# Optimization experiments

Hardware: AMD Instinct MI355X
Metric: run time of the kernel (lower is better)

Reference implementation:

```python
import jax, jax.numpy as jnp
import numpy as np

D_MODEL = 256; D_STATE = 64; D_CONV = 4; EXPAND = 2; HEADDIM = 64; CHUNK = 64
D_INNER = EXPAND * D_MODEL          # 512
NHEADS = D_INNER // HEADDIM         # 8
D_IN_PROJ = 2 * D_INNER + 2 * D_STATE + NHEADS   # 1160
CONV_DIM = D_INNER + 2 * D_STATE    # 640
OBS_DIM = 3; T = 4096; BK = 32; K = 4


def setup_inputs() -> dict:
    key = jax.random.key(0)
    ks = jax.random.split(key, 8)
    f = jnp.float32
    return {
        "obs": jax.random.normal(ks[0], (T, BK, OBS_DIM), f),
        "W_in": jax.random.normal(ks[1], (D_MODEL, OBS_DIM), f) * 0.1,
        "b_in": jnp.zeros((D_MODEL,), f),
        "in_proj_w": jax.random.normal(ks[2], (D_IN_PROJ, D_MODEL), f) * 0.02,
        "conv_w": jax.random.normal(ks[3], (CONV_DIM, D_CONV), f) * 0.2,
        "conv_b": jnp.zeros((CONV_DIM,), f),
        "dt_bias": jax.random.normal(ks[4], (NHEADS,), f) * 0.1,
        "A_log": jnp.log(jnp.arange(1, NHEADS + 1, dtype=f)),
        "D_param": jnp.ones((NHEADS,), f),
        "norm_w": jnp.ones((D_INNER,), f),
        "out_proj_w": jax.random.normal(ks[5], (D_MODEL, D_INNER), f) * 0.02,
        "head": jnp.zeros((1,), f),
        "log_tau": jnp.zeros((1,), f),
        "k": K,
    }


def segsum(x):
    """Stable segment-sum: x (..., T) -> (..., T, T) lower-triangular cumulative sums."""
    L = x.shape[-1]
    x = jnp.broadcast_to(x[..., None], (*x.shape, L))
    x = jnp.where(jnp.tril(jnp.ones((L, L), bool), -1), x, 0.0)
    s = jnp.cumsum(x, axis=-2)
    return jnp.where(jnp.tril(jnp.ones((L, L), bool), 0), s, -jnp.inf)


def ssd(x, A, B, C, chunk):
    """Mamba2 SSD. x:(b,l,h,p) A:(b,l,h) B,C:(b,l,n). Returns y:(b,l,h,p), final state."""
    b, l, h, p = x.shape
    c = l // chunk
    x = x.reshape(b, c, chunk, h, p)
    A = A.reshape(b, c, chunk, h).transpose(0, 3, 1, 2)        # (b,h,c,l)
    B = B.reshape(b, c, chunk, -1)
    C = C.reshape(b, c, chunk, -1)
    A_cs = jnp.cumsum(A, axis=-1)                              # (b,h,c,l)
    Lmat = jnp.exp(segsum(A))                                  # (b,h,c,l,s)
    Y_diag = jnp.einsum('bcln,bcsn,bhcls,bcshp->bclhp', C, B, Lmat, x)
    decay_states = jnp.exp(A_cs[..., -1:] - A_cs)              # (b,h,c,l)
    states = jnp.einsum('bcln,bhcl,bclhp->bchpn', B, decay_states, x)
    states = jnp.concatenate([jnp.zeros_like(states[:, :1]), states], axis=1)
    decay_chunk = jnp.exp(segsum(jnp.pad(A_cs[..., -1], ((0, 0), (0, 0), (1, 0)))))
    new_states = jnp.einsum('bhzc,bchpn->bzhpn', decay_chunk, states)
    states, final = new_states[:, :-1], new_states[:, -1]
    Y_off = jnp.einsum('bcln,bchpn,bhcl->bclhp', C, states, jnp.exp(A_cs))
    return (Y_diag + Y_off).reshape(b, l, h, p), final


def reference(obs, W_in, b_in, in_proj_w, conv_w, conv_b, dt_bias, A_log, D_param,
              norm_w, out_proj_w, head, log_tau, k):
    Tt, Bk, _ = obs.shape
    x = obs @ W_in.T + b_in                        # (T,Bk,d_model)  input linear
    u = jnp.transpose(x, (1, 0, 2))                # (Bk,T,d_model)
    zxbcdt = u @ in_proj_w.T                       # (Bk,T,d_in_proj)
    z = zxbcdt[..., :D_INNER]
    xBC = zxbcdt[..., D_INNER:D_INNER + CONV_DIM]
    dt = jax.nn.softplus(zxbcdt[..., D_INNER + CONV_DIM:] + dt_bias)   # (B,T,h)
    # causal depthwise conv1d + silu (kernel D_CONV)
    xp = jnp.pad(xBC, ((0, 0), (D_CONV - 1, 0), (0, 0)))
    conv = conv_b
    for i in range(D_CONV):
        conv = conv + xp[:, i:i + Tt, :] * conv_w[:, i]
    xBC = jax.nn.silu(conv)
    xs = xBC[..., :D_INNER].reshape(Bk, Tt, NHEADS, HEADDIM)
    Bm = xBC[..., D_INNER:D_INNER + D_STATE]
    Cm = xBC[..., D_INNER + D_STATE:]
    A = -jnp.exp(A_log)                            # (h,)
    y, _final = ssd(xs * dt[..., None], A * dt, Bm, Cm, CHUNK)
    y = y + xs * D_param[None, None, :, None]
    y = y.reshape(Bk, Tt, D_INNER)
    # gated RMSNorm
    y = y * jax.nn.silu(z)
    y = y * jax.lax.rsqrt(jnp.mean(y * y, axis=-1, keepdims=True) + 1e-5) * norm_w
    y = y @ out_proj_w.T                           # (Bk,T,d_model)
    y = jnp.transpose(y, (1, 0, 2))                # (T,Bk,d_model)
    q = jnp.sum(y, axis=-1) * jax.nn.softplus(head)  # (T,Bk)
    q = q.reshape(Tt, -1, k)
    logits = q / jnp.exp(log_tau)
    return (q, logits)
```

## Files before the change

kernel.cpp:

```cpp
#include <hip/hip_runtime.h>

typedef __attribute__((ext_vector_type(8))) short short8;
typedef __attribute__((ext_vector_type(8))) unsigned short ushort8;
typedef __attribute__((ext_vector_type(4))) float f32x4;
typedef __attribute__((ext_vector_type(2))) unsigned int uint2v;

#define OFF_WC 0
#define OFF_BC 3480
#define OFF_W3 4640
#define OFF_TB 12320
#define OFF_NW 14880
#define OFF_Y_BYTES 262144

__device__ __forceinline__ unsigned short f2bf(float f){
  unsigned int u = __float_as_uint(f);
  u = (u + 0x7FFFu + ((u >> 16) & 1u)) >> 16;
  return (unsigned short)u;
}
__device__ __forceinline__ float bf2f(unsigned short h){
  return __uint_as_float(((unsigned int)h) << 16);
}
__device__ __forceinline__ unsigned int cvtpk(float lo, float hi){
  unsigned int r;
  asm("v_cvt_pk_bf16_f32 %0, %1, %2" : "=v"(r) : "v"(lo), "v"(hi));
  return r;
}
__device__ __forceinline__ float softplusf_(float x){
  return (x > 15.f) ? x : log1pf(__expf(x));
}
__device__ __forceinline__ float siluf_(float x){
  return x * __fdividef(1.f, 1.f + __expf(-x));
}

#define SW(row_, col_) ((row_)*64 + ((col_) ^ (((row_)&7)<<3)))

__global__ void prep1_kernel(const float* __restrict__ ipw,
                             const float* __restrict__ W_in,
                             const float* __restrict__ b_in,
                             float* __restrict__ wsf){
  int gw = (blockIdx.x*256 + threadIdx.x) >> 6;
  int lane = threadIdx.x & 63;
  if (gw >= 1160) return;
  const float* row = ipw + (size_t)gw*256;
  float a0=0.f,a1=0.f,a2=0.f,ab=0.f;
  #pragma unroll
  for (int m = lane; m < 256; m += 64){
    float w = row[m];
    a0 = fmaf(w, W_in[m*3+0], a0);
    a1 = fmaf(w, W_in[m*3+1], a1);
    a2 = fmaf(w, W_in[m*3+2], a2);
    ab = fmaf(w, b_in[m], ab);
  }
  #pragma unroll
  for (int o=32;o;o>>=1){
    a0 += __shfl_xor(a0,o); a1 += __shfl_xor(a1,o);
    a2 += __shfl_xor(a2,o); ab += __shfl_xor(ab,o);
  }
  if (lane==0){
    wsf[OFF_WC + gw*3+0]=a0; wsf[OFF_WC + gw*3+1]=a1; wsf[OFF_WC + gw*3+2]=a2;
    wsf[OFF_BC + gw]=ab;
  }
}

__global__ void prep2_kernel(const float* __restrict__ conv_w,
                             const float* __restrict__ norm_w,
                             const float* __restrict__ out_proj_w,
                             float* __restrict__ wsf){
  int r = blockIdx.x*256 + threadIdx.x;
  if (r < 640){
    float bc = wsf[OFF_BC + 512 + r];
    #pragma unroll
    for (int i=0;i<4;i++){
      float cw = conv_w[r*4+i];
      wsf[OFF_TB + r*4+i] = cw*bc;
      wsf[OFF_W3 + r*12 + i*3+0] = cw * wsf[OFF_WC + (512+r)*3+0];
      wsf[OFF_W3 + r*12 + i*3+1] = cw * wsf[OFF_WC + (512+r)*3+1];
      wsf[OFF_W3 + r*12 + i*3+2] = cw * wsf[OFF_WC + (512+r)*3+2];
    }
  }
  if (r < 512){
    float s=0.f;
    for (int m=0;m<256;m++) s += out_proj_w[(size_t)m*512 + r];
    wsf[OFF_NW + r] = norm_w[r]*s;
  }
}

__global__ __launch_bounds__(1024, 4) void ssd_kernel(
    const float* __restrict__ obs, const float* __restrict__ conv_b,
    const float* __restrict__ dt_bias, const float* __restrict__ A_log,
    const float* __restrict__ D_param, const float* __restrict__ wsf,
    unsigned short* __restrict__ Yg)
{
  __shared__ __align__(16) unsigned short BsT[2][4096];
  __shared__ __align__(16) unsigned short CsT[2][4096];
  __shared__ __align__(16) unsigned short XDTt[2][4096];
  __shared__ __align__(16) unsigned short BDTt[2][4096];
  __shared__ __align__(16) unsigned short MmD[2][4096];
  __shared__ __align__(16) unsigned short SbD[2][4096];
  __shared__ __align__(16) unsigned short OW[2][64*40];
  __shared__ __align__(16) float acs_l[4096];
  __shared__ __align__(16) float dt_l[4096];
  __shared__ float CBe[192];

  const int tid  = threadIdx.x;
  const int b    = blockIdx.x >> 3;
  const int h    = blockIdx.x & 7;
  const int lane = tid & 63;
  const int wid  = tid >> 6;
  const int ln15 = lane & 15;
  const int quad = (lane >> 4) & 3;
  const int quad4 = quad*4, quad8 = quad*8;
  const int tm   = wid >> 2, tn = wid & 3;
  const int am    = tm*16 + ln15;
  const int bn    = tn*16 + ln15;
  const int rbase = tm*16 + quad4;

  unsigned short* const W3T = &MmD[0][0];

  for (int i = tid; i < 192*40; i += 1024){
    int lc = i/40, k = i - lc*40;
    unsigned short v = 0;
    if (k < 12){
      int ch = (lc<64) ? h*64+lc : 448+lc;
      v = f2bf(wsf[OFF_W3 + ch*12 + k]);
    }
    W3T[i] = v;
  }
  for (int i = tid; i < 2*64*28; i += 1024){
    int r = i/28; (&OW[0][0])[r*40 + 12 + (i - r*28)] = 0;
  }
  if (tid < 192){
    int ch = (tid<64) ? h*64+tid : 448+tid;
    float s = conv_b[ch];
    #pragma unroll
    for (int i=0;i<4;i++) s += wsf[OFF_TB + ch*4 + i];
    CBe[tid] = s;
  }
  const float Wd0 = wsf[OFF_WC+(1152+h)*3+0], Wd1 = wsf[OFF_WC+(1152+h)*3+1],
              Wd2 = wsf[OFF_WC+(1152+h)*3+2];
  const float bdt = wsf[OFF_BC + 1152 + h] + dt_bias[h];
  const float A_h = -__expf(A_log[h]);
  const float Dh  = D_param[h];
  for (int cc = wid; cc < 64; cc += 16){
    int t = cc*64 + lane;
    const float* ob = obs + (size_t)t*96 + b*3;
    float draw = bdt + Wd0*ob[0] + Wd1*ob[1] + Wd2*ob[2];
    float dtv = softplusf_(draw);
    float a = A_h * dtv;
    #pragma unroll
    for (int o=1;o<64;o<<=1){
      float u = __shfl_up(a, o);
      if (lane >= o) a += u;
    }
    dt_l[t]  = dtv;
    acs_l[t] = a;
  }

  auto PREFOW = [&](int cn){
    if (tid < 768){
      int tt_ = tid/12, ij = tid - tt_*12;
      int i = ij/3, j = ij - i*3;
      int ts = cn*64 + tt_ - 3 + i;
      OW[cn&1][tt_*40 + ij] = (ts >= 0) ? f2bf(obs[(size_t)ts*96 + b*3 + j])
                                        : (unsigned short)0;
    }
  };
  PREFOW(0);
  PREFOW(1);
  __syncthreads();

  short8 afrag1[2], afrag2[2];
  float  cbe1[2][4], cbe2[2];
  #pragma unroll
  for (int e=0;e<2;e++){
    const int idx = wid*2+e;
    const int ct1 = 4 + (idx & 7);
    afrag1[e] = *(const short8*)&W3T[(ct1*16 + ln15)*40 + quad8];
    #pragma unroll
    for (int r=0;r<4;r++) cbe1[e][r] = CBe[ct1*16 + quad4 + r];
    const int ct2 = idx & 7;
    afrag2[e] = *(const short8*)&W3T[(ct2*16 + ln15)*40 + quad8];
    cbe2[e] = CBe[ct2*16 + ln15];
  }

  auto STAGE = [&](int cn, int ps){
    unsigned short* Bp  = &BsT[ps][0];
    unsigned short* Cp  = &CsT[ps][0];
    unsigned short* Xp  = &XDTt[ps][0];
    unsigned short* BDp = &BDTt[ps][0];
    const int tW0 = cn*64;
    const float At_ = acs_l[tW0 + 63];
    #pragma unroll
    for (int e=0;e<2;e++){
      const int idx = wid*2+e;
      const int tt  = idx >> 3;
      const short8 owf = *(const short8*)&OW[cn&1][(tt*16 + ln15)*40 + quad8];
      {
        const int ct1 = 4 + (idx & 7);
        const int chb = ct1*16 + quad4;
        const int t_  = tt*16 + ln15;
        f32x4 z0 = {0.f,0.f,0.f,0.f};
        f32x4 g = __builtin_amdgcn_mfma_f32_16x16x32_bf16(afrag1[e], owf, z0, 0,0,0);
        float v[4];
        #pragma unroll
        for (int r=0;r<4;r++){
          float pre = g[r] + cbe1[e][r];
          if (cn==0 && tt==0 && ln15 < 3){
            int chg = 448 + chb + r;
            #pragma unroll
            for (int i2=0;i2<3;i2++) if (i2 < 3-ln15) pre -= wsf[OFF_TB + chg*4 + i2];
          }
          v[r] = siluf_(pre);
        }
        if (ct1 < 8){
          *(uint2v*)&Bp[SW(t_, chb-64)]  = (uint2v){cvtpk(v[0],v[1]), cvtpk(v[2],v[3])};
        } else {
          *(uint2v*)&Cp[SW(t_, chb-128)] = (uint2v){cvtpk(v[0],v[1]), cvtpk(v[2],v[3])};
        }
      }
      {
        const int ct2 = idx & 7;
        const int ch2 = ct2*16 + ln15;
        const int tb2 = tt*16 + quad4;
        f32x4 z0 = {0.f,0.f,0.f,0.f};
        f32x4 g = __builtin_amdgcn_mfma_f32_16x16x32_bf16(owf, afrag2[e], z0, 0,0,0);
        float v[4];
        #pragma unroll
        for (int r=0;r<4;r++){
          float pre = g[r] + cbe2[e];
          if (cn==0 && tt==0 && quad==0 && r<3){
            int chg = (ch2<64) ? h*64+ch2 : 448+ch2;
            #pragma unroll
            for (int i2=0;i2<3;i2++) if (i2 < 3-r) pre -= wsf[OFF_TB + chg*4 + i2];
          }
          v[r] = siluf_(pre);
        }
        if (ct2 < 4){
          f32x4 dv = *(const f32x4*)&dt_l[tW0 + tb2];
          *(uint2v*)&Xp[SW(ch2, tb2)] =
            (uint2v){cvtpk(v[0]*dv[0], v[1]*dv[1]), cvtpk(v[2]*dv[2], v[3]*dv[3])};
        } else {
          f32x4 av4 = *(const f32x4*)&acs_l[tW0 + tb2];
          float m0 = v[0]*__expf(At_-av4[0]), m1 = v[1]*__expf(At_-av4[1]);
          float m2 = v[2]*__expf(At_-av4[2]), m3 = v[3]*__expf(At_-av4[3]);
          *(uint2v*)&BDp[SW(ch2-64, tb2)] = (uint2v){cvtpk(m0,m1), cvtpk(m2,m3)};
        }
      }
    }
  };

  auto D_PHASE = [&](int cn, int ps){
    const int tc = cn*64;
    short8 cf[2];
    #pragma unroll
    for (int k=0;k<2;k++) cf[k] = *(const short8*)&CsT[ps][SW(bn, k*32+quad8)];
    f32x4 g2 = {0.f,0.f,0.f,0.f};
    #pragma unroll
    for (int k=0;k<2;k++){
      const short8 av = *(const short8*)&BsT[ps][SW(am, k*32+quad8)];
      g2 = __builtin_amdgcn_mfma_f32_16x16x32_bf16(av, cf[k], g2, 0, 0, 0);
    }
    f32x4 acsS = *(const f32x4*)&acs_l[tc + rbase];
    f32x4 dtS  = *(const f32x4*)&dt_l[tc + rbase];
    float acl  = acs_l[tc + bn];
    float mv[4];
    #pragma unroll
    for (int r=0;r<4;r++){
      int s = rbase + r;
      float m_ = (bn >= s) ? g2[r]*__expf(acl - acsS[r]) : 0.f;
      if (bn == s) m_ += __fdividef(Dh, dtS[r]);
      mv[r] = m_;
    }
    *(uint2v*)&MmD[ps][SW(bn, rbase)] = (uint2v){cvtpk(mv[0],mv[1]), cvtpk(mv[2],mv[3])};
  };

  STAGE(0, 0);
  __syncthreads();

  D_PHASE(0, 0);
  *(uint2v*)&SbD[0][SW(bn, rbase)] = (uint2v){0u, 0u};
  __syncthreads();

  f32x4 sreg = {0.f,0.f,0.f,0.f};

  for (int c = 0; c < 64; ++c){
    const int t0 = c*64;
    const int ps = c & 1;

    if (c < 63) STAGE(c+1, ps^1);
    if (c < 62) PREFOW(c+2);
    __syncthreads();

    {
      short8 mfr[2], ccf[2], xbn[2];
      #pragma unroll
      for (int k=0;k<2;k++){
        int kb = k*32 + quad8;
        mfr[k] = *(const short8*)&MmD[ps][SW(bn, kb)];
        ccf[k] = *(const short8*)&CsT[ps][SW(bn, kb)];
        xbn[k] = *(const short8*)&XDTt[ps][SW(bn, kb)];
      }
      f32x4 y  = {0.f,0.f,0.f,0.f};
      f32x4 yo = {0.f,0.f,0.f,0.f};
      #pragma unroll
      for (int k=0;k<2;k++){
        int kb = k*32 + quad8;
        const short8 xa = *(const short8*)&XDTt[ps][SW(am, kb)];
        y = __builtin_amdgcn_mfma_f32_16x16x32_bf16(xa, mfr[k], y, 0, 0, 0);
      }
      #pragma unroll
      for (int k=0;k<2;k++){
        int kb = k*32 + quad8;
        const short8 sa = *(const short8*)&SbD[ps][SW(am, kb)];
        yo = __builtin_amdgcn_mfma_f32_16x16x32_bf16(sa, ccf[k], yo, 0, 0, 0);
      }
      float eAcl  = __expf(acs_l[t0 + bn]);
      float eAtot = __expf(acs_l[t0 + 63]);
      uint2v pk = {cvtpk(y[0]+eAcl*yo[0], y[1]+eAcl*yo[1]),
                   cvtpk(y[2]+eAcl*yo[2], y[3]+eAcl*yo[3])};
      *(uint2v*)&Yg[((size_t)(b*4096 + t0 + bn))*512 + h*64 + rbase] = pk;
      #pragma unroll
      for (int r=0;r<4;r++) sreg[r] *= eAtot;
      #pragma unroll
      for (int k=0;k<2;k++){
        int kb = k*32 + quad8;
        const short8 ba = *(const short8*)&BDTt[ps][SW(am, kb)];
        sreg = __builtin_amdgcn_mfma_f32_16x16x32_bf16(ba, xbn[k], sreg, 0, 0, 0);
      }
      if (c < 63){
        D_PHASE(c+1, ps^1);
        *(uint2v*)&SbD[ps^1][SW(bn, rbase)] =
          (uint2v){cvtpk(sreg[0],sreg[1]), cvtpk(sreg[2],sreg[3])};
      }
    }
    __syncthreads();
  }
}

__global__ __launch_bounds__(256) void final_kernel(
    const unsigned short* __restrict__ Yg, const float* __restrict__ obs,
    const float* __restrict__ wsf, const float* __restrict__ head,
    const float* __restrict__ log_tau, float* __restrict__ out)
{
  int tid = threadIdx.x;
  int wv = tid >> 6, lane = tid & 63;
  float zw0[8], zw1[8], zw2[8], zb[8], znw[8];
  #pragma unroll
  for (int u=0;u<8;u++){
    int ch = lane*8 + u;
    zw0[u] = wsf[OFF_WC + ch*3+0];
    zw1[u] = wsf[OFF_WC + ch*3+1];
    zw2[u] = wsf[OFF_WC + ch*3+2];
    zb[u]  = wsf[OFF_BC + ch];
    znw[u] = wsf[OFF_NW + ch];
  }
  float hsc  = softplusf_(head[0]);
  float itau = __expf(-log_tau[0]);
  int base = blockIdx.x*64 + wv*16;
  for (int rr=0; rr<16; ++rr){
    int row = base + rr;
    int bb = row >> 12, t = row & 4095;
    const float* ob = obs + (size_t)t*96 + bb*3;
    float o0=ob[0], o1=ob[1], o2=ob[2];
    ushort8 yv = *(const ushort8*)&Yg[(size_t)row*512 + lane*8];
    float s2=0.f, sq=0.f;
    #pragma unroll
    for (int u=0;u<8;u++){
      float yf = bf2f(yv[u]);
      float z  = zb[u] + zw0[u]*o0 + zw1[u]*o1 + zw2[u]*o2;
      float yg = yf * siluf_(z);
      s2 = fmaf(yg, yg, s2);
      sq = fmaf(yg, znw[u], sq);
    }
    #pragma unroll
    for (int o=32;o;o>>=1){ s2 += __shfl_xor(s2,o); sq += __shfl_xor(sq,o); }
    if (lane==0){
      float rms = rsqrtf(s2*(1.f/512.f) + 1e-5f);
      float q = sq * rms * hsc;
      out[(size_t)t*32 + bb] = q;
      out[131072 + (size_t)t*32 + bb] = q * itau;
    }
  }
}

extern "C" void kernel_launch(void* const* d_in, const int* in_sizes, int n_in,
                              void* d_out, int out_size, void* d_ws, size_t ws_size,
                              hipStream_t stream) {
  (void)in_sizes; (void)n_in; (void)out_size; (void)ws_size;
  const float* obs        = (const float*)d_in[0];
  const float* W_in       = (const float*)d_in[1];
  const float* b_in       = (const float*)d_in[2];
  const float* in_proj_w  = (const float*)d_in[3];
  const float* conv_w     = (const float*)d_in[4];
  const float* conv_b     = (const float*)d_in[5];
  const float* dt_bias    = (const float*)d_in[6];
  const float* A_log      = (const float*)d_in[7];
  const float* D_param    = (const float*)d_in[8];
  const float* norm_w     = (const float*)d_in[9];
  const float* out_proj_w = (const float*)d_in[10];
  const float* head       = (const float*)d_in[11];
  const float* log_tau    = (const float*)d_in[12];
  float* wsf = (float*)d_ws;
  unsigned short* Yg = (unsigned short*)((char*)d_ws + OFF_Y_BYTES);
  float* out = (float*)d_out;

  prep1_kernel<<<290, 256, 0, stream>>>(in_proj_w, W_in, b_in, wsf);
  prep2_kernel<<<3, 256, 0, stream>>>(conv_w, norm_w, out_proj_w, wsf);
  ssd_kernel<<<256, 1024, 0, stream>>>(obs, conv_b, dt_bias, A_log, D_param, wsf, Yg);
  final_kernel<<<2048, 256, 0, stream>>>(Yg, obs, wsf, head, log_tau, out);
}
```

Before: 395.2 us.

## Software-pipeline SSD chunk loop with triple-buffered stages and per-chunk dt ring

The SSD kernel drops the upfront full-sequence dt/cumsum pass and computes dt, cumulative A and decay per chunk into a small ring, produced two chunks ahead by one wave. Stage buffers become triple-buffered so STAGE, D_PHASE and the output/state update of different chunks run in one iteration, leaving one barrier per chunk. Conv-edge handling is folded into the MFMA by adding tap-bias columns with a validity indicator, which removes the branchy first-chunk correction. The final kernel gets larger blocks that stage weights and obs in shared memory, so fewer blocks launch. The cost is more LDS use and more index bookkeeping in exchange for less serialization and fewer barriers.

```diff
diff --git a/kernel.cpp b/kernel.cpp
--- a/kernel.cpp
+++ b/kernel.cpp
@@ -91,15 +91,13 @@
     const float* __restrict__ D_param, const float* __restrict__ wsf,
     unsigned short* __restrict__ Yg)
 {
-  __shared__ __align__(16) unsigned short BsT[2][4096];
-  __shared__ __align__(16) unsigned short CsT[2][4096];
-  __shared__ __align__(16) unsigned short XDTt[2][4096];
-  __shared__ __align__(16) unsigned short BDTt[2][4096];
+  __shared__ __align__(16) unsigned short SG[3][4][4096];
   __shared__ __align__(16) unsigned short MmD[2][4096];
   __shared__ __align__(16) unsigned short SbD[2][4096];
   __shared__ __align__(16) unsigned short OW[2][64*40];
-  __shared__ __align__(16) float acs_l[4096];
-  __shared__ __align__(16) float dt_l[4096];
+  __shared__ __align__(16) float ring_acs[4][64];
+  __shared__ __align__(16) float ring_dt[4][64];
+  __shared__ __align__(16) float ring_dcy[4][64];
   __shared__ float CBe[192];
 
   const int tid  = threadIdx.x;
@@ -117,32 +115,14 @@
 
   unsigned short* const W3T = &MmD[0][0];
 
-  for (int i = tid; i < 192*40; i += 1024){
-    int lc = i/40, k = i - lc*40;
-    unsigned short v = 0;
-    if (k < 12){
-      int ch = (lc<64) ? h*64+lc : 448+lc;
-      v = f2bf(wsf[OFF_W3 + ch*12 + k]);
-    }
-    W3T[i] = v;
-  }
-  for (int i = tid; i < 2*64*28; i += 1024){
-    int r = i/28; (&OW[0][0])[r*40 + 12 + (i - r*28)] = 0;
-  }
-  if (tid < 192){
-    int ch = (tid<64) ? h*64+tid : 448+tid;
-    float s = conv_b[ch];
-    #pragma unroll
-    for (int i=0;i<4;i++) s += wsf[OFF_TB + ch*4 + i];
-    CBe[tid] = s;
-  }
   const float Wd0 = wsf[OFF_WC+(1152+h)*3+0], Wd1 = wsf[OFF_WC+(1152+h)*3+1],
               Wd2 = wsf[OFF_WC+(1152+h)*3+2];
   const float bdt = wsf[OFF_BC + 1152 + h] + dt_bias[h];
   const float A_h = -__expf(A_log[h]);
   const float Dh  = D_param[h];
-  for (int cc = wid; cc < 64; cc += 16){
-    int t = cc*64 + lane;
+
+  auto RING = [&](int cn){
+    int t = cn*64 + lane;
     const float* ob = obs + (size_t)t*96 + b*3;
     float draw = bdt + Wd0*ob[0] + Wd1*ob[1] + Wd2*ob[2];
     float dtv = softplusf_(draw);
@@ -152,21 +132,47 @@
       float u = __shfl_up(a, o);
       if (lane >= o) a += u;
     }
-    dt_l[t]  = dtv;
-    acs_l[t] = a;
-  }
+    float At = __shfl(a, 63);
+    int s = cn & 3;
+    ring_dt[s][lane]  = dtv;
+    ring_acs[s][lane] = a;
+    ring_dcy[s][lane] = __expf(At - a);
+  };
 
   auto PREFOW = [&](int cn){
-    if (tid < 768){
-      int tt_ = tid/12, ij = tid - tt_*12;
-      int i = ij/3, j = ij - i*3;
-      int ts = cn*64 + tt_ - 3 + i;
-      OW[cn&1][tt_*40 + ij] = (ts >= 0) ? f2bf(obs[(size_t)ts*96 + b*3 + j])
-                                        : (unsigned short)0;
-    }
+    int row = tid >> 4, col = tid & 15;
+    unsigned short val;
+    if (col < 12){
+      int i = col/3, j = col - i*3;
+      int ts = cn*64 + row - 3 + i;
+      val = (ts >= 0) ? f2bf(obs[(size_t)ts*96 + b*3 + j]) : (unsigned short)0;
+    } else {
+      int ts = cn*64 + row - 3 + (col - 12);
+      val = (ts >= 0) ? (unsigned short)0x3F80 : (unsigned short)0;
+    }
+    OW[cn&1][row*40 + col] = val;
   };
+
+  for (int i = tid; i < 192*40; i += 1024){
+    int lc = i/40, k = i - lc*40;
+    int ch = (lc<64) ? h*64+lc : 448+lc;
+    float v = 0.f;
+    if (k < 12)       v = wsf[OFF_W3 + ch*12 + k];
+    else if (k < 16)  v = wsf[OFF_TB + ch*4 + (k-12)];
+    W3T[i] = f2bf(v);
+  }
+  for (int i = tid; i < 2048; i += 1024){
+    int bf = i >> 10, r2 = (i >> 4) & 63, c2 = 16 + (i & 15);
+    OW[bf][r2*40 + c2] = 0;
+  }
+  if (tid < 192){
+    int ch = (tid<64) ? h*64+tid : 448+tid;
+    CBe[tid] = conv_b[ch];
+  }
+  if (wid >= 14) RING(wid - 14);
   PREFOW(0);
   PREFOW(1);
+  ((uint2v*)&SbD[0][0])[tid] = (uint2v){0u, 0u};
   __syncthreads();
 
   short8 afrag1[2], afrag2[2];
@@ -183,13 +189,12 @@
     cbe2[e] = CBe[ct2*16 + ln15];
   }
 
-  auto STAGE = [&](int cn, int ps){
-    unsigned short* Bp  = &BsT[ps][0];
-    unsigned short* Cp  = &CsT[ps][0];
-    unsigned short* Xp  = &XDTt[ps][0];
-    unsigned short* BDp = &BDTt[ps][0];
-    const int tW0 = cn*64;
-    const float At_ = acs_l[tW0 + 63];
+  auto STAGE = [&](int cn, int bi){
+    unsigned short* Bp  = &SG[bi][0][0];
+    unsigned short* Cp  = &SG[bi][1][0];
+    unsigned short* Xp  = &SG[bi][2][0];
+    unsigned short* BDp = &SG[bi][3][0];
+    const int s = cn & 3;
     #pragma unroll
     for (int e=0;e<2;e++){
       const int idx = wid*2+e;
@@ -203,15 +208,7 @@
         f32x4 g = __builtin_amdgcn_mfma_f32_16x16x32_bf16(afrag1[e], owf, z0, 0,0,0);
         float v[4];
         #pragma unroll
-        for (int r=0;r<4;r++){
-          float pre = g[r] + cbe1[e][r];
-          if (cn==0 && tt==0 && ln15 < 3){
-            int chg = 448 + chb + r;
-            #pragma unroll
-            for (int i2=0;i2<3;i2++) if (i2 < 3-ln15) pre -= wsf[OFF_TB + chg*4 + i2];
-          }
-          v[r] = siluf_(pre);
-        }
+        for (int r=0;r<4;r++) v[r] = siluf_(g[r] + cbe1[e][r]);
         if (ct1 < 8){
           *(uint2v*)&Bp[SW(t_, chb-64)]  = (uint2v){cvtpk(v[0],v[1]), cvtpk(v[2],v[3])};
         } else {
@@ -226,112 +223,95 @@
         f32x4 g = __builtin_amdgcn_mfma_f32_16x16x32_bf16(owf, afrag2[e], z0, 0,0,0);
         float v[4];
         #pragma unroll
-        for (int r=0;r<4;r++){
-          float pre = g[r] + cbe2[e];
-          if (cn==0 && tt==0 && quad==0 && r<3){
-            int chg = (ch2<64) ? h*64+ch2 : 448+ch2;
-            #pragma unroll
-            for (int i2=0;i2<3;i2++) if (i2 < 3-r) pre -= wsf[OFF_TB + chg*4 + i2];
-          }
-          v[r] = siluf_(pre);
-        }
+        for (int r=0;r<4;r++) v[r] = siluf_(g[r] + cbe2[e]);
         if (ct2 < 4){
-          f32x4 dv = *(const f32x4*)&dt_l[tW0 + tb2];
+          f32x4 dv = *(const f32x4*)&ring_dt[s][tb2];
           *(uint2v*)&Xp[SW(ch2, tb2)] =
             (uint2v){cvtpk(v[0]*dv[0], v[1]*dv[1]), cvtpk(v[2]*dv[2], v[3]*dv[3])};
         } else {
-          f32x4 av4 = *(const f32x4*)&acs_l[tW0 + tb2];
-          float m0 = v[0]*__expf(At_-av4[0]), m1 = v[1]*__expf(At_-av4[1]);
-          float m2 = v[2]*__expf(At_-av4[2]), m3 = v[3]*__expf(At_-av4[3]);
-          *(uint2v*)&BDp[SW(ch2-64, tb2)] = (uint2v){cvtpk(m0,m1), cvtpk(m2,m3)};
+          f32x4 cv = *(const f32x4*)&ring_dcy[s][tb2];
+          *(uint2v*)&BDp[SW(ch2-64, tb2)] =
+            (uint2v){cvtpk(v[0]*cv[0], v[1]*cv[1]), cvtpk(v[2]*cv[2], v[3]*cv[3])};
         }
       }
     }
   };
 
-  auto D_PHASE = [&](int cn, int ps){
-    const int tc = cn*64;
+  auto D_PHASE = [&](int cn){
+    const int bi = cn % 3, s = cn & 3, ms = cn & 1;
     short8 cf[2];
     #pragma unroll
-    for (int k=0;k<2;k++) cf[k] = *(const short8*)&CsT[ps][SW(bn, k*32+quad8)];
+    for (int k=0;k<2;k++) cf[k] = *(const short8*)&SG[bi][1][SW(bn, k*32+quad8)];
     f32x4 g2 = {0.f,0.f,0.f,0.f};
     #pragma unroll
     for (int k=0;k<2;k++){
-      const short8 av = *(const short8*)&BsT[ps][SW(am, k*32+quad8)];
+      const short8 av = *(const short8*)&SG[bi][0][SW(am, k*32+quad8)];
       g2 = __builtin_amdgcn_mfma_f32_16x16x32_bf16(av, cf[k], g2, 0, 0, 0);
     }
-    f32x4 acsS = *(const f32x4*)&acs_l[tc + rbase];
-    f32x4 dtS  = *(const f32x4*)&dt_l[tc + rbase];
-    float acl  = acs_l[tc + bn];
+    f32x4 acsS = *(const f32x4*)&ring_acs[s][rbase];
+    f32x4 dtS  = *(const f32x4*)&ring_dt[s][rbase];
+    float acl  = ring_acs[s][bn];
     float mv[4];
     #pragma unroll
     for (int r=0;r<4;r++){
-      int s = rbase + r;
-      float m_ = (bn >= s) ? g2[r]*__expf(acl - acsS[r]) : 0.f;
-      if (bn == s) m_ += __fdividef(Dh, dtS[r]);
+      int sr = rbase + r;
+      float m_ = (bn >= sr) ? g2[r]*__expf(acl - acsS[r]) : 0.f;
+      if (bn == sr) m_ += __fdividef(Dh, dtS[r]);
       mv[r] = m_;
     }
-    *(uint2v*)&MmD[ps][SW(bn, rbase)] = (uint2v){cvtpk(mv[0],mv[1]), cvtpk(mv[2],mv[3])};
+    *(uint2v*)&MmD[ms][SW(bn, rbase)] = (uint2v){cvtpk(mv[0],mv[1]), cvtpk(mv[2],mv[3])};
   };
 
   STAGE(0, 0);
   __syncthreads();
 
-  D_PHASE(0, 0);
-  *(uint2v*)&SbD[0][SW(bn, rbase)] = (uint2v){0u, 0u};
-  __syncthreads();
-
   f32x4 sreg = {0.f,0.f,0.f,0.f};
 
-  for (int c = 0; c < 64; ++c){
-    const int t0 = c*64;
-    const int ps = c & 1;
-
-    if (c < 63) STAGE(c+1, ps^1);
-    if (c < 62) PREFOW(c+2);
-    __syncthreads();
-
-    {
+  for (int c = 0; c <= 64; ++c){
+    if (wid == 15 && c <= 61) RING(c+2);
+    if (c <= 61) PREFOW(c+2);
+    if (c <= 62) STAGE(c+1, (c+1)%3);
+    if (c <= 63) D_PHASE(c);
+    if (c >= 1){
+      const int j = c-1;
+      const int bi = j % 3, ms = j & 1, s = j & 3;
       short8 mfr[2], ccf[2], xbn[2];
       #pragma unroll
       for (int k=0;k<2;k++){
         int kb = k*32 + quad8;
-        mfr[k] = *(const short8*)&MmD[ps][SW(bn, kb)];
-        ccf[k] = *(const short8*)&CsT[ps][SW(bn, kb)];
-        xbn[k] = *(const short8*)&XDTt[ps][SW(bn, kb)];
+        mfr[k] = *(const short8*)&MmD[ms][SW(bn, kb)];
+        ccf[k] = *(const short8*)&SG[bi][1][SW(bn, kb)];
+        xbn[k] = *(const short8*)&SG[bi][2][SW(bn, kb)];
       }
       f32x4 y  = {0.f,0.f,0.f,0.f};
       f32x4 yo = {0.f,0.f,0.f,0.f};
       #pragma unroll
       for (int k=0;k<2;k++){
         int kb = k*32 + quad8;
-        const short8 xa = *(const short8*)&XDTt[ps][SW(am, kb)];
+        const short8 xa = *(const short8*)&SG[bi][2][SW(am, kb)];
         y = __builtin_amdgcn_mfma_f32_16x16x32_bf16(xa, mfr[k], y, 0, 0, 0);
       }
       #pragma unroll
       for (int k=0;k<2;k++){
         int kb = k*32 + quad8;
-        const short8 sa = *(const short8*)&SbD[ps][SW(am, kb)];
+        const short8 sa = *(const short8*)&SbD[ms][SW(am, kb)];
         yo = __builtin_amdgcn_mfma_f32_16x16x32_bf16(sa, ccf[k], yo, 0, 0, 0);
       }
-      float eAcl  = __expf(acs_l[t0 + bn]);
-      float eAtot = __expf(acs_l[t0 + 63]);
+      float eAcl  = __expf(ring_acs[s][bn]);
+      float eAtot = __expf(ring_acs[s][63]);
       uint2v pk = {cvtpk(y[0]+eAcl*yo[0], y[1]+eAcl*yo[1]),
                    cvtpk(y[2]+eAcl*yo[2], y[3]+eAcl*yo[3])};
-      *(uint2v*)&Yg[((size_t)(b*4096 + t0 + bn))*512 + h*64 + rbase] = pk;
+      *(uint2v*)&Yg[((size_t)(b*4096 + j*64 + bn))*512 + h*64 + rbase] = pk;
       #pragma unroll
       for (int r=0;r<4;r++) sreg[r] *= eAtot;
       #pragma unroll
       for (int k=0;k<2;k++){
         int kb = k*32 + quad8;
-        const short8 ba = *(const short8*)&BDTt[ps][SW(am, kb)];
+        const short8 ba = *(const short8*)&SG[bi][3][SW(am, kb)];
         sreg = __builtin_amdgcn_mfma_f32_16x16x32_bf16(ba, xbn[k], sreg, 0, 0, 0);
       }
-      if (c < 63){
-        D_PHASE(c+1, ps^1);
-        *(uint2v*)&SbD[ps^1][SW(bn, rbase)] =
-          (uint2v){cvtpk(sreg[0],sreg[1]), cvtpk(sreg[2],sreg[3])};
-      }
+      *(uint2v*)&SbD[ms^1][SW(bn, rbase)] =
+        (uint2v){cvtpk(sreg[0],sreg[1]), cvtpk(sreg[2],sreg[3])};
     }
     __syncthreads();
   }
@@ -342,27 +322,38 @@
     const float* __restrict__ wsf, const float* __restrict__ head,
     const float* __restrict__ log_tau, float* __restrict__ out)
 {
-  int tid = threadIdx.x;
-  int wv = tid >> 6, lane = tid & 63;
+  __shared__ float w0_s[512], w1_s[512], w2_s[512], bz_s[512], nw_s[512];
+  __shared__ float obs_s[256*3];
+  const int tid = threadIdx.x;
+  const int bb = blockIdx.x >> 4;
+  const int t0 = (blockIdx.x & 15) << 8;
+  for (int i = tid; i < 512; i += 256){
+    w0_s[i] = wsf[OFF_WC + i*3+0];
+    w1_s[i] = wsf[OFF_WC + i*3+1];
+    w2_s[i] = wsf[OFF_WC + i*3+2];
+    bz_s[i] = wsf[OFF_BC + i];
+    nw_s[i] = wsf[OFF_NW + i];
+  }
+  for (int i = tid; i < 768; i += 256){
+    int tt = i/3, j = i - tt*3;
+    obs_s[i] = obs[(size_t)(t0+tt)*96 + bb*3 + j];
+  }
+  __syncthreads();
+  const int wv = tid >> 6, lane = tid & 63;
   float zw0[8], zw1[8], zw2[8], zb[8], znw[8];
   #pragma unroll
   for (int u=0;u<8;u++){
     int ch = lane*8 + u;
-    zw0[u] = wsf[OFF_WC + ch*3+0];
-    zw1[u] = wsf[OFF_WC + ch*3+1];
-    zw2[u] = wsf[OFF_WC + ch*3+2];
-    zb[u]  = wsf[OFF_BC + ch];
-    znw[u] = wsf[OFF_NW + ch];
+    zw0[u] = w0_s[ch]; zw1[u] = w1_s[ch]; zw2[u] = w2_s[ch];
+    zb[u] = bz_s[ch]; znw[u] = nw_s[ch];
   }
   float hsc  = softplusf_(head[0]);
   float itau = __expf(-log_tau[0]);
-  int base = blockIdx.x*64 + wv*16;
-  for (int rr=0; rr<16; ++rr){
-    int row = base + rr;
-    int bb = row >> 12, t = row & 4095;
-    const float* ob = obs + (size_t)t*96 + bb*3;
-    float o0=ob[0], o1=ob[1], o2=ob[2];
-    ushort8 yv = *(const ushort8*)&Yg[(size_t)row*512 + lane*8];
+  for (int rr = 0; rr < 64; ++rr){
+    int tl = wv*64 + rr;
+    int t  = t0 + tl;
+    float o0 = obs_s[tl*3+0], o1 = obs_s[tl*3+1], o2 = obs_s[tl*3+2];
+    ushort8 yv = *(const ushort8*)&Yg[((size_t)bb*4096 + t)*512 + lane*8];
     float s2=0.f, sq=0.f;
     #pragma unroll
     for (int u=0;u<8;u++){
@@ -407,5 +398,5 @@
   prep1_kernel<<<290, 256, 0, stream>>>(in_proj_w, W_in, b_in, wsf);
   prep2_kernel<<<3, 256, 0, stream>>>(conv_w, norm_w, out_proj_w, wsf);
   ssd_kernel<<<256, 1024, 0, stream>>>(obs, conv_b, dt_bias, A_log, D_param, wsf, Yg);
-  final_kernel<<<2048, 256, 0, stream>>>(Yg, obs, wsf, head, log_tau, out);
-}
+  final_kernel<<<512, 256, 0, stream>>>(Yg, obs, wsf, head, log_tau, out);
+}
```

Measured after the change: 431.4 us. +9.2%, slower.
